# Optimization experiments

Hardware: AMD Instinct MI355X
Metric: run time of the kernel (lower is better)

The kernel has to match this reference:

```python
import jax, jax.numpy as jnp
import numpy as np

B, POMO, PROB, EMB, H, D = 64, 200, 200, 512, 16, 32
SQRT_EMB = 22.627416997969522  # sqrt(512)
CLIP = 10.0


def _heads(x):
    # (b, n, H*D) -> (b, H, n, D)
    b, n, _ = x.shape
    return x.reshape(b, n, H, D).transpose(0, 2, 1, 3)


def setup_inputs() -> dict:
    key = jax.random.key(0)
    ks = jax.random.split(key, 10)
    s = 1.0 / np.sqrt(EMB)
    return {
        "encoded_nodes": jax.random.normal(ks[0], (B, PROB + 1, EMB), jnp.float32),
        "encoded_q1": jax.random.normal(ks[1], (B, POMO, EMB), jnp.float32),
        "encoded_last_node": jax.random.normal(ks[2], (B, POMO, EMB), jnp.float32),
        "ninf_mask": jnp.zeros((B, POMO, PROB), jnp.float32),
        "Wq_first": jax.random.normal(ks[3], (EMB, H * D), jnp.float32) * s,
        "Wq_last": jax.random.normal(ks[4], (EMB, H * D), jnp.float32) * s,
        "Wk": jax.random.normal(ks[5], (EMB, H * D), jnp.float32) * s,
        "Wv": jax.random.normal(ks[6], (EMB, H * D), jnp.float32) * s,
        "Wc": jax.random.normal(ks[7], (H * D, EMB), jnp.float32) * s,
        "bc": jax.random.normal(ks[8], (EMB,), jnp.float32) * 0.01,
    }


def reference(encoded_nodes, encoded_q1, encoded_last_node, ninf_mask,
              Wq_first, Wq_last, Wk, Wv, Wc, bc):
    # set_kv
    k = _heads(encoded_nodes @ Wk)            # (b, H, prob+1, D)
    v = _heads(encoded_nodes @ Wv)            # (b, H, prob+1, D)
    single_head_key = encoded_nodes[:, :-1]   # (b, prob, emb)
    # set_q1 + forward queries
    q = _heads(encoded_q1 @ Wq_first) + _heads(encoded_last_node @ Wq_last)  # (b, H, pomo, D)
    # masked multi-head attention; mask padded with a zero column for the depot/last node
    mask3 = jnp.concatenate([ninf_mask, jnp.zeros((B, POMO, 1), ninf_mask.dtype)], axis=-1)
    score = jnp.einsum('bhnd,bhmd->bhnm', q, k) / jnp.sqrt(jnp.float32(D))
    weights = jax.nn.softmax(score + mask3[:, None, :, :], axis=-1)
    out = jnp.einsum('bhnm,bhmd->bhnd', weights, v)        # (b, H, pomo, D)
    out_concat = out.transpose(0, 2, 1, 3).reshape(B, POMO, H * D)
    mh_atten_out = out_concat @ Wc + bc                    # (b, pomo, emb)
    # single-head pointer score with tanh clipping
    score2 = jnp.einsum('bne,bpe->bnp', mh_atten_out, single_head_key) / SQRT_EMB
    score_masked = CLIP * jnp.tanh(score2) + ninf_mask
    return jax.nn.softmax(score_masked, axis=2)            # (b, pomo, prob)
```

## Files before the change

### kernel.cpp

```cpp
#include <hip/hip_runtime.h>
#include <cstdint>
#include <cstddef>

typedef _Float16 f16;
typedef f16 f16x4 __attribute__((ext_vector_type(4)));
typedef f16 f16x8 __attribute__((ext_vector_type(8)));
typedef float f32x4 __attribute__((ext_vector_type(4)));

#define NB    64
#define NPOMO 200
#define NNODE 201
#define NEMB  512
#define NH    16
#define ND    32
#define VTSTR 208

__device__ __forceinline__ void gload16(const void* g, void* l) {
  __builtin_amdgcn_global_load_lds((const __attribute__((address_space(1))) void*)g,
                                   (__attribute__((address_space(3))) void*)l, 16, 0, 0);
}


__global__ void prep_kernel(const float* __restrict__ enc, const float* __restrict__ q1,
                            const float* __restrict__ ql, const float* __restrict__ Wk,
                            const float* __restrict__ Wv, const float* __restrict__ Wqf,
                            const float* __restrict__ Wql, const float* __restrict__ Wc,
                            f16* __restrict__ Xnh, f16* __restrict__ Qcat,
                            f16* __restrict__ wkvT, f16* __restrict__ wqT,
                            f16* __restrict__ wcT) {
  const int bx = blockIdx.x;
  const int tid = threadIdx.x;
  if (bx < 6432) {
    int i = bx * 256 + tid;
    if (i < 1646592) {
      float4 v = ((const float4*)enc)[i];
      f16x4 h = {(f16)v.x, (f16)v.y, (f16)v.z, (f16)v.w};
      ((f16x4*)Xnh)[i] = h;
    }
  } else if (bx < 19232) {
    int i = (bx - 6432) * 256 + tid;
    int row = i >> 8;
    int g = i & 255;
    const float* src = (g < 128) ? (q1 + (size_t)row * 512 + g * 4)
                                 : (ql + (size_t)row * 512 + (g - 128) * 4);
    float4 v = *(const float4*)src;
    f16x4 h = {(f16)v.x, (f16)v.y, (f16)v.z, (f16)v.w};
    ((f16x4*)Qcat)[i] = h;
  } else {
    int i = (bx - 19232) * 256 + tid;
    if (i < 524288) {
      int j = i >> 9, k = i & 511;
      float v = (j < 512) ? Wk[(size_t)k * 512 + j] : Wv[(size_t)k * 512 + (j - 512)];
      wkvT[i] = (f16)v;
    } else if (i < 1048576) {
      int t = i - 524288;
      int j = t >> 10, k = t & 1023;
      float v = (k < 512) ? Wqf[(size_t)k * 512 + j] : Wql[(size_t)(k - 512) * 512 + j];
      wqT[t] = (f16)v;
    } else if (i < 1310720) {
      int t = i - 1048576;
      int j = t >> 9, k = t & 511;
      wcT[t] = (f16)Wc[(size_t)k * 512 + j];
    }
  }
}


__device__ __forceinline__ void gemm_body(
    const f16* __restrict__ A, const f16* __restrict__ B, f16* __restrict__ C,
    const float* __restrict__ bias, int M, int N, int K, int m0, int n0,
    f16* As, f16* Bs, f16* __restrict__ vtp) {
  const int tid = threadIdx.x;
  const int wave = tid >> 6, lane = tid & 63;
  const int qd = lane >> 4, c = lane & 15;
  const int wm = wave >> 1, wn = wave & 1;
  const int srow = lane >> 3, sj = lane & 7;

  f32x4 acc[4][4];
#pragma unroll
  for (int i = 0; i < 4; ++i)
#pragma unroll
    for (int j = 0; j < 4; ++j) acc[i][j] = (f32x4){0.f, 0.f, 0.f, 0.f};

  for (int kc = 0; kc < K; kc += 64) {
#pragma unroll
    for (int i = 0; i < 4; ++i) {
      int row = wave * 32 + i * 8 + srow;
      int gr = m0 + row; if (gr >= M) gr = M - 1;
      int gj = sj ^ (row & 7);
      gload16(A + (size_t)gr * K + kc + gj * 8, As + row * 64 + sj * 8);
    }
#pragma unroll
    for (int i = 0; i < 4; ++i) {
      int row = wave * 32 + i * 8 + srow;
      int gj = sj ^ (row & 7);
      gload16(B + (size_t)(n0 + row) * K + kc + gj * 8, Bs + row * 64 + sj * 8);
    }
    __syncthreads();
#pragma unroll
    for (int kk = 0; kk < 2; ++kk) {
      f16x8 af[4], bf[4];
#pragma unroll
      for (int t = 0; t < 4; ++t) {
        int ra = wm * 64 + t * 16 + c;
        af[t] = *(const f16x8*)(As + ra * 64 + (((kk * 4 + qd) ^ (ra & 7)) * 8));
        int rb = wn * 64 + t * 16 + c;
        bf[t] = *(const f16x8*)(Bs + rb * 64 + (((kk * 4 + qd) ^ (rb & 7)) * 8));
      }
#pragma unroll
      for (int mt = 0; mt < 4; ++mt)
#pragma unroll
        for (int nt = 0; nt < 4; ++nt)
          acc[mt][nt] = __builtin_amdgcn_mfma_f32_16x16x32_f16(af[mt], bf[nt], acc[mt][nt], 0, 0, 0);
    }
    __syncthreads();
  }

#pragma unroll
  for (int mt = 0; mt < 4; ++mt) {
#pragma unroll
    for (int nt = 0; nt < 4; ++nt) {
      int col = n0 + wn * 64 + nt * 16 + c;
      float bv = bias ? bias[col] : 0.0f;
#pragma unroll
      for (int r = 0; r < 4; ++r) {
        int row = m0 + wm * 64 + mt * 16 + qd * 4 + r;
        if (row < M) {
          f16 hv = (f16)(acc[mt][nt][r] + bv);
          if (!vtp) {
            C[(size_t)row * N + col] = hv;
          } else if (col < 512) {
            C[(size_t)row * 512 + col] = hv;
          } else {
            int bb = row / 201, node = row - bb * 201;
            int hd = col - 512;
            vtp[(((size_t)(bb * NH) + (hd >> 5)) * 32 + (hd & 31)) * VTSTR + node] = hv;
          }
        }
      }
    }
  }
}

__global__ __launch_bounds__(256, 2) void gemm_proj(
    const f16* __restrict__ Xnh, const f16* __restrict__ WkvT, f16* __restrict__ Kp,
    f16* __restrict__ VT, const f16* __restrict__ Qcat, const f16* __restrict__ WqT,
    f16* __restrict__ Qp) {
  __shared__ f16 As[128 * 64];
  __shared__ f16 Bs[128 * 64];
  const int bx = blockIdx.x;
  if (bx < 808) {
    gemm_body(Xnh, WkvT, Kp, nullptr, 12864, 1024, 512, (bx % 101) * 128, (bx / 101) * 128, As, Bs, VT);
  } else {
    int t = bx - 808;
    gemm_body(Qcat, WqT, Qp, nullptr, 12800, 512, 1024, (t % 100) * 128, (t / 100) * 128, As, Bs, nullptr);
  }
}

__global__ __launch_bounds__(256, 2) void gemm_wc(
    const f16* __restrict__ Oc, const f16* __restrict__ WcT, f16* __restrict__ mhb,
    const float* __restrict__ bc) {
  __shared__ f16 As[128 * 64];
  __shared__ f16 Bs[128 * 64];
  const int bx = blockIdx.x;
  gemm_body(Oc, WcT, mhb, bc, 12800, 512, 512, (bx % 100) * 128, (bx / 100) * 128, As, Bs, nullptr);
}


__global__ __launch_bounds__(256, 4) void attn_kernel(
    const f16* __restrict__ Qp, const f16* __restrict__ Kp,
    const f16* __restrict__ VT, const float* __restrict__ mask,
    f16* __restrict__ Oc) {
  const int bid = blockIdx.x;
  const int hg = bid & 3;
  const int rt = (bid >> 2) % 13;
  const int b = bid / 52;
  const int wave = threadIdx.x >> 6, lane = threadIdx.x & 63;
  const int qd = lane >> 4, c = lane & 15;
  const int h = hg * 4 + wave;

  const int r0 = rt * 16;
  const int qrow = min(r0 + c, 199);
  const float scale = 0.17677669529663687f;

  f16x8 aq = *(const f16x8*)(Qp + ((size_t)(b * NPOMO + qrow)) * 512 + h * 32 + qd * 8);

  f32x4 s[13];
#pragma unroll
  for (int nt = 0; nt < 13; ++nt) {
    int node = nt * 16 + c; if (node > 200) node = 200;
    f16x8 ak = *(const f16x8*)(Kp + ((size_t)(b * NNODE + node)) * 512 + h * 32 + qd * 8);
    f32x4 z = (f32x4){0.f, 0.f, 0.f, 0.f};
    s[nt] = __builtin_amdgcn_mfma_f32_16x16x32_f16(ak, aq, z, 0, 0, 0);
  }

  float mx = -3e38f;
#pragma unroll
  for (int nt = 0; nt < 13; ++nt) {
    const int col0 = nt * 16 + qd * 4;
    float4 mv = make_float4(0.f, 0.f, 0.f, 0.f);
    if (col0 < 200)
      mv = *(const float4*)(mask + ((size_t)b * NPOMO + qrow) * 200 + col0);
#pragma unroll
    for (int r = 0; r < 4; ++r) {
      int node = col0 + r;
      float v;
      if (node > 200)      v = -3e38f;
      else if (node == 200) v = s[nt][r] * scale;
      else                  v = s[nt][r] * scale + ((const float*)&mv)[r];
      s[nt][r] = v;
      mx = fmaxf(mx, v);
    }
  }
  mx = fmaxf(mx, __shfl_xor(mx, 16));
  mx = fmaxf(mx, __shfl_xor(mx, 32));

  float sm = 0.f;
  f16x4 pf[13];
#pragma unroll
  for (int nt = 0; nt < 13; ++nt) {
    f16x4 p4;
#pragma unroll
    for (int r = 0; r < 4; ++r) {
      float p = __expf(s[nt][r] - mx);
      sm += p;
      p4[r] = (f16)p;
    }
    pf[nt] = p4;
  }
  sm += __shfl_xor(sm, 16);
  sm += __shfl_xor(sm, 32);
  const float inv = 1.0f / sm;

  const f16* vbase = VT + ((size_t)(b * NH + h)) * 32 * VTSTR;
  f32x4 o0 = (f32x4){0.f, 0.f, 0.f, 0.f};
  f32x4 o1 = (f32x4){0.f, 0.f, 0.f, 0.f};
#pragma unroll
  for (int nt = 0; nt < 13; ++nt) {
    const int nb = nt * 16 + qd * 4;
    f16x4 av0 = *(const f16x4*)(vbase + c * VTSTR + nb);
    f16x4 av1 = *(const f16x4*)(vbase + (c + 16) * VTSTR + nb);
    o0 = __builtin_amdgcn_mfma_f32_16x16x16f16(av0, pf[nt], o0, 0, 0, 0);
    o1 = __builtin_amdgcn_mfma_f32_16x16x16f16(av1, pf[nt], o1, 0, 0, 0);
  }

  const int row = r0 + c;
  if (row < 200) {
    f16* dst = Oc + ((size_t)(b * NPOMO + row)) * 512 + h * 32 + qd * 4;
    f16x4 w0 = {(f16)(o0[0] * inv), (f16)(o0[1] * inv), (f16)(o0[2] * inv), (f16)(o0[3] * inv)};
    f16x4 w1 = {(f16)(o1[0] * inv), (f16)(o1[1] * inv), (f16)(o1[2] * inv), (f16)(o1[3] * inv)};
    *(f16x4*)dst = w0;
    *(f16x4*)(dst + 16) = w1;
  }
}


__global__ __launch_bounds__(256, 4) void final_kernel(
    const f16* __restrict__ mh, const f16* __restrict__ Xnh,
    const float* __restrict__ mask, float* __restrict__ out) {
  __shared__ float xmax[4][16];
  __shared__ float xsum[4][16];
  const int b = blockIdx.x / 13;
  const int tile = blockIdx.x % 13;
  const int r0 = tile * 16;
  const int tid = threadIdx.x;
  const int wave = tid >> 6, lane = tid & 63;
  const int qd = lane >> 4, c = lane & 15;

  const int nt0 = (wave == 0) ? 0 : (3 * wave + 1);
  const int cnt = (wave == 0) ? 4 : 3;

  const int qrow = min(r0 + c, 199);
  const size_t rbase = ((size_t)(b * NPOMO + qrow)) * 512;

  size_t abase[4];
#pragma unroll
  for (int i = 0; i < 4; ++i) {
    int nt = nt0 + i;
    int nd = nt * 16 + c; if (nd > 200) nd = 200;
    abase[i] = ((size_t)(b * NNODE + nd)) * 512;
  }

  f32x4 acc[4];
#pragma unroll
  for (int i = 0; i < 4; ++i) acc[i] = (f32x4){0.f, 0.f, 0.f, 0.f};

#pragma unroll 4
  for (int kc = 0; kc < 512; kc += 32) {
    f16x8 bq = *(const f16x8*)(mh + rbase + kc + qd * 8);
#pragma unroll
    for (int i = 0; i < 4; ++i) {
      if (i < cnt) {
        f16x8 a = *(const f16x8*)(Xnh + abase[i] + kc + qd * 8);
        acc[i] = __builtin_amdgcn_mfma_f32_16x16x32_f16(a, bq, acc[i], 0, 0, 0);
      }
    }
  }

  const float invS = 1.0f / 22.627416997969522f;
  float mx = -3e38f;
#pragma unroll
  for (int i = 0; i < 4; ++i) {
    if (i >= cnt) break;
    const int nt = nt0 + i;
    const int col0 = nt * 16 + qd * 4;
    float4 mv = make_float4(0.f, 0.f, 0.f, 0.f);
    if (col0 < 200)
      mv = *(const float4*)(mask + ((size_t)b * NPOMO + qrow) * 200 + col0);
#pragma unroll
    for (int r = 0; r < 4; ++r) {
      int node = col0 + r;
      float v;
      if (node < 200) {
        float t = __expf(2.0f * acc[i][r] * invS);
        float th = 1.0f - 2.0f / (t + 1.0f);
        v = 10.0f * th + ((const float*)&mv)[r];
      } else {
        v = -3e38f;
      }
      acc[i][r] = v;
      mx = fmaxf(mx, v);
    }
  }
  mx = fmaxf(mx, __shfl_xor(mx, 16));
  mx = fmaxf(mx, __shfl_xor(mx, 32));
  if (lane < 16) xmax[wave][lane] = mx;
  __syncthreads();
  mx = fmaxf(fmaxf(xmax[0][c], xmax[1][c]), fmaxf(xmax[2][c], xmax[3][c]));

  float sm = 0.f;
#pragma unroll
  for (int i = 0; i < 4; ++i) {
    if (i >= cnt) break;
#pragma unroll
    for (int r = 0; r < 4; ++r) {
      float p = __expf(acc[i][r] - mx);
      acc[i][r] = p;
      sm += p;
    }
  }
  sm += __shfl_xor(sm, 16);
  sm += __shfl_xor(sm, 32);
  if (lane < 16) xsum[wave][lane] = sm;
  __syncthreads();
  const float tot = xsum[0][c] + xsum[1][c] + xsum[2][c] + xsum[3][c];
  const float inv = 1.0f / tot;

  const int row = r0 + c;
  if (row < 200) {
#pragma unroll
    for (int i = 0; i < 4; ++i) {
      if (i >= cnt) break;
      const int col0 = (nt0 + i) * 16 + qd * 4;
      if (col0 < 200) {
        float4 o;
        o.x = acc[i][0] * inv; o.y = acc[i][1] * inv;
        o.z = acc[i][2] * inv; o.w = acc[i][3] * inv;
        *(float4*)(out + ((size_t)b * NPOMO + row) * 200 + col0) = o;
      }
    }
  }
}


extern "C" void kernel_launch(void* const* d_in, const int* in_sizes, int n_in,
                              void* d_out, int out_size, void* d_ws, size_t ws_size,
                              hipStream_t stream) {
  (void)in_sizes; (void)n_in; (void)out_size; (void)ws_size;
  const float* enc   = (const float*)d_in[0];
  const float* q1    = (const float*)d_in[1];
  const float* qlast = (const float*)d_in[2];
  const float* mask  = (const float*)d_in[3];
  const float* Wqf   = (const float*)d_in[4];
  const float* Wql   = (const float*)d_in[5];
  const float* Wk    = (const float*)d_in[6];
  const float* Wv    = (const float*)d_in[7];
  const float* Wc    = (const float*)d_in[8];
  const float* bc    = (const float*)d_in[9];
  float* out = (float*)d_out;

  char* ws = (char*)d_ws;
  f16* Xnh  = (f16*)(ws + 0);
  f16* Qcat = (f16*)(ws + 13172736);
  f16* WkvT = (f16*)(ws + 39387136);
  f16* WqT  = (f16*)(ws + 40435712);
  f16* WcT  = (f16*)(ws + 41484288);
  f16* Kp   = (f16*)(ws + 42008576);
  f16* VT   = (f16*)(ws + 55181312);
  f16* Qp   = (f16*)(ws + 68812800);
  f16* Oc   = (f16*)(ws + 81920000);
  f16* mhb  = (f16*)(ws + 95027200);

  hipLaunchKernelGGL(prep_kernel, dim3(24352), dim3(256), 0, stream,
                     enc, q1, qlast, Wk, Wv, Wqf, Wql, Wc, Xnh, Qcat, WkvT, WqT, WcT);
  hipLaunchKernelGGL(gemm_proj, dim3(1208), dim3(256), 0, stream,
                     Xnh, WkvT, Kp, VT, Qcat, WqT, Qp);
  hipLaunchKernelGGL(attn_kernel, dim3(3328), dim3(256), 0, stream, Qp, Kp, VT, mask, Oc);
  hipLaunchKernelGGL(gemm_wc, dim3(400), dim3(256), 0, stream, Oc, WcT, mhb, bc);
  hipLaunchKernelGGL(final_kernel, dim3(832), dim3(256), 0, stream, mhb, Xnh, mask, out);
}
```

Baseline: 296.2 us.

## Widen projection GEMM tiles to 128x256 with 512-thread blocks

The projection GEMM now uses 512-thread blocks computing 128x256 output tiles, with 8 waves arranged 2x4, instead of 256-thread blocks doing 128x128 tiles. This halves the grid and reuses each A tile across twice as many columns, cutting global and LDS traffic for A. It also schedules the longer K=1024 Q-projection blocks first. The cost is more shared memory per block (48KB) and a fatter block, which may reduce occupancy and lengthen the tail.

```diff
diff --git a/kernel.cpp b/kernel.cpp
--- a/kernel.cpp
+++ b/kernel.cpp
@@ -66,15 +66,13 @@
 }
 
 
-__device__ __forceinline__ void gemm_body(
+__device__ __forceinline__ void gemm_body512(
     const f16* __restrict__ A, const f16* __restrict__ B, f16* __restrict__ C,
-    const float* __restrict__ bias, int M, int N, int K, int m0, int n0,
-    f16* As, f16* Bs, f16* __restrict__ vtp) {
+    int M, int K, int m0, int n0, f16* As, f16* Bs, f16* __restrict__ vtp) {
   const int tid = threadIdx.x;
   const int wave = tid >> 6, lane = tid & 63;
   const int qd = lane >> 4, c = lane & 15;
-  const int wm = wave >> 1, wn = wave & 1;
-  const int srow = lane >> 3, sj = lane & 7;
+  const int wm = wave >> 2, wn = wave & 3;
 
   f32x4 acc[4][4];
 #pragma unroll
@@ -84,17 +82,19 @@
 
   for (int kc = 0; kc < K; kc += 64) {
 #pragma unroll
-    for (int i = 0; i < 4; ++i) {
-      int row = wave * 32 + i * 8 + srow;
+    for (int i = 0; i < 2; ++i) {
+      int id = tid + i * 512;
+      int row = id >> 3, sj = id & 7;
       int gr = m0 + row; if (gr >= M) gr = M - 1;
       int gj = sj ^ (row & 7);
-      gload16(A + (size_t)gr * K + kc + gj * 8, As + row * 64 + sj * 8);
+      gload16(A + (size_t)gr * K + kc + gj * 8, As + id * 8);
     }
 #pragma unroll
     for (int i = 0; i < 4; ++i) {
-      int row = wave * 32 + i * 8 + srow;
+      int id = tid + i * 512;
+      int row = id >> 3, sj = id & 7;
       int gj = sj ^ (row & 7);
-      gload16(B + (size_t)(n0 + row) * K + kc + gj * 8, Bs + row * 64 + sj * 8);
+      gload16(B + (size_t)(n0 + row) * K + kc + gj * 8, Bs + id * 8);
     }
     __syncthreads();
 #pragma unroll
@@ -121,14 +121,13 @@
 #pragma unroll
     for (int nt = 0; nt < 4; ++nt) {
       int col = n0 + wn * 64 + nt * 16 + c;
-      float bv = bias ? bias[col] : 0.0f;
 #pragma unroll
       for (int r = 0; r < 4; ++r) {
         int row = m0 + wm * 64 + mt * 16 + qd * 4 + r;
         if (row < M) {
-          f16 hv = (f16)(acc[mt][nt][r] + bv);
+          f16 hv = (f16)acc[mt][nt][r];
           if (!vtp) {
-            C[(size_t)row * N + col] = hv;
+            C[(size_t)row * 512 + col] = hv;
           } else if (col < 512) {
             C[(size_t)row * 512 + col] = hv;
           } else {
@@ -142,18 +141,84 @@
   }
 }
 
-__global__ __launch_bounds__(256, 2) void gemm_proj(
+__global__ __launch_bounds__(512, 4) void gemm_proj(
     const f16* __restrict__ Xnh, const f16* __restrict__ WkvT, f16* __restrict__ Kp,
     f16* __restrict__ VT, const f16* __restrict__ Qcat, const f16* __restrict__ WqT,
     f16* __restrict__ Qp) {
   __shared__ f16 As[128 * 64];
-  __shared__ f16 Bs[128 * 64];
+  __shared__ f16 Bs[256 * 64];
   const int bx = blockIdx.x;
-  if (bx < 808) {
-    gemm_body(Xnh, WkvT, Kp, nullptr, 12864, 1024, 512, (bx % 101) * 128, (bx / 101) * 128, As, Bs, VT);
+  if (bx < 200) {
+    gemm_body512(Qcat, WqT, Qp, 12800, 1024, (bx % 100) * 128, (bx / 100) * 256, As, Bs, nullptr);
   } else {
-    int t = bx - 808;
-    gemm_body(Qcat, WqT, Qp, nullptr, 12800, 512, 1024, (t % 100) * 128, (t / 100) * 128, As, Bs, nullptr);
+    int t = bx - 200;
+    gemm_body512(Xnh, WkvT, Kp, 12864, 512, (t % 101) * 128, (t / 101) * 256, As, Bs, VT);
+  }
+}
+
+
+__device__ __forceinline__ void gemm_body(
+    const f16* __restrict__ A, const f16* __restrict__ B, f16* __restrict__ C,
+    const float* __restrict__ bias, int M, int N, int K, int m0, int n0,
+    f16* As, f16* Bs) {
+  const int tid = threadIdx.x;
+  const int wave = tid >> 6, lane = tid & 63;
+  const int qd = lane >> 4, c = lane & 15;
+  const int wm = wave >> 1, wn = wave & 1;
+  const int srow = lane >> 3, sj = lane & 7;
+
+  f32x4 acc[4][4];
+#pragma unroll
+  for (int i = 0; i < 4; ++i)
+#pragma unroll
+    for (int j = 0; j < 4; ++j) acc[i][j] = (f32x4){0.f, 0.f, 0.f, 0.f};
+
+  for (int kc = 0; kc < K; kc += 64) {
+#pragma unroll
+    for (int i = 0; i < 4; ++i) {
+      int row = wave * 32 + i * 8 + srow;
+      int gr = m0 + row; if (gr >= M) gr = M - 1;
+      int gj = sj ^ (row & 7);
+      gload16(A + (size_t)gr * K + kc + gj * 8, As + row * 64 + sj * 8);
+    }
+#pragma unroll
+    for (int i = 0; i < 4; ++i) {
+      int row = wave * 32 + i * 8 + srow;
+      int gj = sj ^ (row & 7);
+      gload16(B + (size_t)(n0 + row) * K + kc + gj * 8, Bs + row * 64 + sj * 8);
+    }
+    __syncthreads();
+#pragma unroll
+    for (int kk = 0; kk < 2; ++kk) {
+      f16x8 af[4], bf[4];
+#pragma unroll
+      for (int t = 0; t < 4; ++t) {
+        int ra = wm * 64 + t * 16 + c;
+        af[t] = *(const f16x8*)(As + ra * 64 + (((kk * 4 + qd) ^ (ra & 7)) * 8));
+        int rb = wn * 64 + t * 16 + c;
+        bf[t] = *(const f16x8*)(Bs + rb * 64 + (((kk * 4 + qd) ^ (rb & 7)) * 8));
+      }
+#pragma unroll
+      for (int mt = 0; mt < 4; ++mt)
+#pragma unroll
+        for (int nt = 0; nt < 4; ++nt)
+          acc[mt][nt] = __builtin_amdgcn_mfma_f32_16x16x32_f16(af[mt], bf[nt], acc[mt][nt], 0, 0, 0);
+    }
+    __syncthreads();
+  }
+
+#pragma unroll
+  for (int mt = 0; mt < 4; ++mt) {
+#pragma unroll
+    for (int nt = 0; nt < 4; ++nt) {
+      int col = n0 + wn * 64 + nt * 16 + c;
+      float bv = bias ? bias[col] : 0.0f;
+#pragma unroll
+      for (int r = 0; r < 4; ++r) {
+        int row = m0 + wm * 64 + mt * 16 + qd * 4 + r;
+        if (row < M) C[(size_t)row * N + col] = (f16)(acc[mt][nt][r] + bv);
+      }
+    }
   }
 }
 
@@ -163,7 +228,7 @@
   __shared__ f16 As[128 * 64];
   __shared__ f16 Bs[128 * 64];
   const int bx = blockIdx.x;
-  gemm_body(Oc, WcT, mhb, bc, 12800, 512, 512, (bx % 100) * 128, (bx / 100) * 128, As, Bs, nullptr);
+  gemm_body(Oc, WcT, mhb, bc, 12800, 512, 512, (bx % 100) * 128, (bx / 100) * 128, As, Bs);
 }
 
 
@@ -393,7 +458,7 @@
 
   hipLaunchKernelGGL(prep_kernel, dim3(24352), dim3(256), 0, stream,
                      enc, q1, qlast, Wk, Wv, Wqf, Wql, Wc, Xnh, Qcat, WkvT, WqT, WcT);
-  hipLaunchKernelGGL(gemm_proj, dim3(1208), dim3(256), 0, stream,
+  hipLaunchKernelGGL(gemm_proj, dim3(604), dim3(512), 0, stream,
                      Xnh, WkvT, Kp, VT, Qcat, WqT, Qp);
   hipLaunchKernelGGL(attn_kernel, dim3(3328), dim3(256), 0, stream, Qp, Kp, VT, mask, Oc);
   hipLaunchKernelGGL(gemm_wc, dim3(400), dim3(256), 0, stream, Oc, WcT, mhb, bc);
```

Measured after the change: 297.5 us. About the same (+0.5%).
